# Kernel tuning notes

Measured on AMD Instinct MI355X. Metric: run time of the kernel, lower is better.

## Reference

```python
import jax, jax.numpy as jnp
import numpy as np

N_QUBITS = 12
N_LAYERS = 4
BATCH = 4096
DIM = 2 ** N_QUBITS  # 4096


def _apply_1q(state, U, q):
    """Apply 2x2 complex gate U to qubit q. state: (B,) + (2,)*n, wire 0 = MSB (axis q+1)."""
    state = jnp.moveaxis(state, q + 1, -1)
    state = state @ U.T
    return jnp.moveaxis(state, -1, q + 1)


def _apply_cnot(state, c, t):
    """CNOT with control c, target t: flip target amplitudes where control bit == 1."""
    flipped = jnp.flip(state, axis=t + 1)
    shape = [2 if i == c + 1 else 1 for i in range(state.ndim)]
    ctrl = jnp.arange(2).reshape(shape)
    return jnp.where(ctrl == 1, flipped, state)


def setup_inputs() -> dict:
    key = jax.random.key(0)
    k1, k2 = jax.random.split(key)
    x = jax.random.normal(k1, (BATCH, DIM), dtype=jnp.float32)
    weights = jax.random.normal(k2, (N_LAYERS, N_QUBITS, 2), dtype=jnp.float32) * 0.1
    return {"x": x, "weights": weights}


def reference(x, weights):
    n, L = N_QUBITS, N_LAYERS
    B = x.shape[0]
    # AmplitudeEmbedding with normalize=True
    norm = jnp.linalg.norm(x, axis=-1, keepdims=True)
    state = (x / norm).astype(jnp.complex64).reshape((B,) + (2,) * n)
    for layer in range(L):
        for q in range(n):
            ty = weights[layer, q, 0]
            tz = weights[layer, q, 1]
            c, s = jnp.cos(ty / 2), jnp.sin(ty / 2)
            em = jnp.exp(-0.5j * tz.astype(jnp.complex64))  # e^{-i tz/2}
            ep = jnp.exp(+0.5j * tz.astype(jnp.complex64))
            # U = RZ(tz) @ RY(ty), fused single 2x2 gate per qubit
            U = jnp.stack([
                jnp.stack([c * em, -s * em]),
                jnp.stack([s * ep, c * ep]),
            ]).astype(jnp.complex64)
            state = _apply_1q(state, U, q)
        for q in range(n - 1):
            state = _apply_cnot(state, q, q + 1)
        if n > 2:
            state = _apply_cnot(state, n - 1, 0)
    probs = jnp.abs(state) ** 2  # (B,) + (2,)*n, float32
    reduce_axes = tuple(range(1, probs.ndim))
    outs = []
    for q in range(n):
        shape = [2 if i == q + 1 else 1 for i in range(probs.ndim)]
        sign = jnp.array([1.0, -1.0], dtype=probs.dtype).reshape(shape)
        outs.append(jnp.sum(probs * sign, axis=reduce_axes))
    return jnp.stack(outs, axis=-1)  # (B, n_qubits) <Z_q> expvals
```

## Files before the change

### kernel.cpp

```cpp
#include <hip/hip_runtime.h>

#define NQ   12
#define DIM  4096
#define NL   4
#define BLK  256

typedef unsigned short u16;
typedef unsigned int   u32;
typedef float f2 __attribute__((ext_vector_type(2)));

struct L12 { u16 b[NQ]; };

static constexpr u32 lap(const L12& A, u32 x){ u32 r=0; for(int p=0;p<NQ;++p) if((x>>p)&1u) r^=A.b[p]; return r; }
static constexpr L12 lcomp(const L12& A, const L12& B){ L12 r{}; for(int p=0;p<NQ;++p) r.b[p]=(u16)lap(A,(u32)B.b[p]); return r; }
static constexpr L12 lident(){ L12 r{}; for(int p=0;p<NQ;++p) r.b[p]=(u16)(1u<<p); return r; }

static constexpr u32 applyT(u32 i){
  i ^= ((i>>0)&1u) << 11;
  for(int q=10;q>=0;--q){ int pc=11-q, pt=10-q; i ^= ((i>>pc)&1u) << pt; }
  return i;
}
static constexpr L12 lT(){ L12 t{}; for(int p=0;p<NQ;++p) t.b[p]=(u16)applyT(1u<<p); return t; }

static constexpr L12 linv(const L12& A){
  u16 v[NQ]; u16 u[NQ];
  for(int p=0;p<NQ;++p){ v[p]=A.b[p]; u[p]=(u16)(1u<<p); }
  for(int t=0;t<NQ;++t){
    int p=t; while(!((v[p]>>t)&1u)) ++p;
    u16 tv=v[p]; v[p]=v[t]; v[t]=tv; u16 tu=u[p]; u[p]=u[t]; u[t]=tu;
    for(int k=0;k<NQ;++k) if(k!=t && ((v[k]>>t)&1u)){ v[k]^=v[t]; u[k]^=u[t]; }
  }
  L12 r{}; for(int p=0;p<NQ;++p) r.b[p]=u[p]; return r;
}
static constexpr L12 ltr(const L12& A){
  L12 r{}; for(int p=0;p<NQ;++p) for(int q=0;q<NQ;++q) if((A.b[p]>>q)&1u) r.b[q]=(u16)(r.b[q]|(1u<<p));
  return r;
}
static constexpr int cpop(u32 v){ int n=0; while(v){ n+=(int)(v&1u); v>>=1; } return n; }

struct Tables {
  u16 cm[12][16];
  u16 wg[12][4];
  u16 sp[12][4];
  u16 wexp[NQ];
};

static constexpr Tables make_tables(){
  Tables tb{};
  const L12 T   = lT();
  const L12 Tit = ltr(linv(T));
  L12 A = lident();
  L12 W = lident();
  for(int l=0;l<NL;++l){
    for(int g=0;g<3;++g){
      const int st = l*3+g;
      u16 mm[4]={0,0,0,0};
      for(int i=0;i<4;++i){ mm[i]=A.b[4*g+i]; tb.wg[st][i]=W.b[4*g+i]; }
      u32 ech[4]={0,0,0,0}; int piv[4]={0,0,0,0};
      for(int i=0;i<4;++i){
        u32 v=mm[i];
        for(int k=0;k<i;++k) if((v>>piv[k])&1u) v^=ech[k];
        int t2=11; while(!((v>>t2)&1u)) --t2;
        piv[i]=t2; ech[i]=v;
      }
      for(int a2=0;a2<4;++a2) for(int b2=a2+1;b2<4;++b2)
        if(piv[b2]<piv[a2]){ int tt=piv[a2]; piv[a2]=piv[b2]; piv[b2]=tt; }
      for(int i=0;i<4;++i) tb.sp[st][i]=(u16)piv[i];
      for(int c=0;c<16;++c){ u32 m=0; for(int i=0;i<4;++i) if((c>>i)&1) m^=mm[i]; tb.cm[st][c]=(u16)m; }
    }
    A = lcomp(A, T);
    W = lcomp(W, Tit);
  }
  for(int p=0;p<NQ;++p) tb.wexp[p]=W.b[p];
  return tb;
}

__device__ constexpr Tables TB = make_tables();

static constexpr u16 UIMG[12] = {1,2,4,8, 3,5,6,7, 9,10,11,13};

static constexpr u32 swz(u32 j){
  u32 f=0;
  for(int k=4;k<12;++k) if((j>>k)&1u) f ^= (u32)UIMG[k];
  return j ^ (f & 15u);
}

struct Derived {
  u32 lane_c[12][8];
  u32 smb[12][4];
  u32 scmb[12][16];
  u32 g0lane[8];
  u32 u11lane[8];
  u32 u11smb[4];
  u16 pm[12];
  u16 mu[12];
};

static constexpr Derived make_derived(){
  const Tables tb = make_tables();
  Derived d{};
  for(int st=0; st<12; ++st){
    bool isp[12]={false,false,false,false,false,false,false,false,false,false,false,false};
    for(int i=0;i<4;++i) isp[tb.sp[st][i]]=true;
    int np[8]; int nn=0;
    for(int p=0;p<12;++p) if(!isp[p]) np[nn++]=p;
    int best=-1;
    for(int ms=0; ms<256; ++ms){
      int pc=0; for(int k=0;k<8;++k) pc+=(ms>>k)&1;
      if(pc!=6) continue;
      u16 bas[4]={0,0,0,0}; int r=0;
      for(int k=0;k<8;++k){
        if(!((ms>>k)&1)) continue;
        u16 x=(u16)(UIMG[np[k]]&15);
        while(x){
          int hb=3; while(!((x>>hb)&1)) --hb;
          if(bas[hb]) x=(u16)(x^bas[hb]);
          else { bas[hb]=x; ++r; x=0; }
        }
      }
      if(r==4){ best=ms; break; }
    }
    if(best<0) best=0x3F;
    int pos[8]; int lo=0, hi=6;
    for(int k=0;k<8;++k){ if((best>>k)&1) pos[lo++]=np[k]; else pos[hi++]=np[k]; }
    for(int k=0;k<8;++k){
      const u32 addr = swz(1u<<pos[k])<<3;
      u32 nib=0;
      for(int i=0;i<4;++i) nib |= (u32)((tb.wg[st][i]>>pos[k])&1u)<<i;
      d.lane_c[st][k] = addr | (nib<<28);
      if(st==0)  d.g0lane[k]  = 1u<<pos[k];
      if(st==11) d.u11lane[k] = 1u<<pos[k];
    }
    for(int i=0;i<4;++i)  d.smb[st][i]  = swz((u32)tb.cm[st][1<<i])<<3;
    for(int c=0;c<16;++c) d.scmb[st][c] = swz((u32)tb.cm[st][c])<<3;
    if(st==11) for(int i=0;i<4;++i) d.u11smb[i] = (u32)tb.cm[11][1<<i];
  }
  for(int q=0;q<12;++q){
    d.pm[q] = tb.wexp[11-q];
    u32 m=0;
    for(int i=0;i<4;++i) m |= (u32)(cpop((u32)tb.cm[11][1u<<i] & (u32)tb.wexp[11-q])&1)<<i;
    d.mu[q]=(u16)m;
  }
  return d;
}

__device__ constexpr Derived DV = make_derived();

template<int ST, bool WITHW>
__device__ __forceinline__ void gates(f2 (&a)[16], const float4* __restrict__ gw){
#pragma unroll
  for(int i=0;i<4;++i){
    const float4 g = gw[ST*4+i];
    const f2 mt = {-g.x, -g.x};
    const f2 sy = { g.y,  g.y};
#pragma unroll
    for(int c=0;c<16;++c){
      if((c>>i)&1) continue;
      const int c1 = c|(1<<i);
      f2 u = __builtin_elementwise_fma(mt, a[c1], a[c]);
      f2 v = __builtin_elementwise_fma(sy, u, a[c1]);
      a[c] = __builtin_elementwise_fma(mt, v, u);
      if(WITHW){
        const float t = fmaf(-g.z, v.y, v.x);
        v.y = fmaf( g.w, t, v.y);
        v.x = fmaf(-g.z, v.y, t);
      }
      a[c1]=v;
    }
  }
}

template<int ST, bool WITHW>
__device__ __forceinline__ void mid_step(const u32* msk, char* lds, const float4* __restrict__ gw){
  u32 acc=0;
#pragma unroll
  for(int k=0;k<8;++k) acc ^= DV.lane_c[ST][k]&msk[k];
  const u32 nib = acc>>28;
  u32 base = acc & 0x0FFFFFFFu;
#pragma unroll
  for(int i=0;i<4;++i) base ^= DV.smb[ST][i] & (0u-((nib>>i)&1u));
  u32 ad[16]; f2 a[16];
#pragma unroll
  for(int c=0;c<16;++c){
    ad[c] = base ^ DV.scmb[ST][c];
    a[c] = *(const f2*)(lds+ad[c]);
  }
  gates<ST,WITHW>(a,gw);
#pragma unroll
  for(int c=0;c<16;++c){ *(f2*)(lds+ad[c]) = a[c]; }
  __syncthreads();
}

__global__ void prep_kernel(const float* __restrict__ w, float4* __restrict__ gw){
  const int t = threadIdx.x;
  if(t < NL*NQ){
    const int l=t/NQ, p=t%NQ, q=(NQ-1)-p;
    const float ty=w[(l*NQ+q)*2+0], tz=w[(l*NQ+q)*2+1];
    gw[t]=make_float4(tanf(0.25f*ty), sinf(0.5f*ty), tanf(0.5f*tz), sinf(tz));
  }
}

__global__ __launch_bounds__(BLK, 5) void qsim_kernel(const float* __restrict__ x,
                                                      const float4* __restrict__ gw,
                                                      float* __restrict__ out)
{
  __shared__ f2 st2[DIM];
  char* lds = (char*)st2;
  const int tid = threadIdx.x;
  const int bb  = blockIdx.x;

  u32 msk[8];
#pragma unroll
  for(int k=0;k<8;++k) msk[k]=0u-((u32)(tid>>k)&1u);

  u32 rep0=0, acc0=0;
#pragma unroll
  for(int k=0;k<8;++k){ rep0 ^= DV.g0lane[k]&msk[k]; acc0 ^= DV.lane_c[0][k]&msk[k]; }
  const u32 base0 = acc0 & 0x0FFFFFFFu;

  f2 a[16];
  const float* xr = x + (size_t)bb*DIM + rep0;
#pragma unroll
  for(int s=0;s<4;++s){
    const float4 v = *reinterpret_cast<const float4*>(xr + 4*s);
    a[4*s+0]=(f2){v.x,0.f}; a[4*s+1]=(f2){v.y,0.f};
    a[4*s+2]=(f2){v.z,0.f}; a[4*s+3]=(f2){v.w,0.f};
  }
  gates<0,true>(a,gw);
#pragma unroll
  for(int c=0;c<16;++c){ *(f2*)(lds + (base0 ^ DV.scmb[0][c])) = a[c]; }
  __syncthreads();

  mid_step<1,true >(msk,lds,gw);
  mid_step<2,true >(msk,lds,gw);
  mid_step<3,true >(msk,lds,gw);
  mid_step<4,true >(msk,lds,gw);
  mid_step<5,true >(msk,lds,gw);
  mid_step<6,true >(msk,lds,gw);
  mid_step<7,true >(msk,lds,gw);
  mid_step<8,true >(msk,lds,gw);
  mid_step<9,false>(msk,lds,gw);
  mid_step<10,false>(msk,lds,gw);

  {
    u32 acc=0, urep=0;
#pragma unroll
    for(int k=0;k<8;++k){ acc ^= DV.lane_c[11][k]&msk[k]; urep ^= DV.u11lane[k]&msk[k]; }
    const u32 nib = acc>>28;
    u32 base = acc & 0x0FFFFFFFu;
#pragma unroll
    for(int i=0;i<4;++i){ const u32 mi=0u-((nib>>i)&1u); base ^= DV.smb[11][i]&mi; urep ^= DV.u11smb[i]&mi; }
#pragma unroll
    for(int c=0;c<16;++c){
      a[c] = *(const f2*)(lds + (base ^ DV.scmb[11][c]));
    }
    gates<11,false>(a,gw);

    float pr[16];
#pragma unroll
    for(int c=0;c<16;++c) pr[c]=fmaf(a[c].x,a[c].x, a[c].y*a[c].y);
#pragma unroll
    for(int b=1;b<16;b<<=1){
#pragma unroll
      for(int c=0;c<16;++c){
        if(c&b) continue;
        const float u=pr[c], v=pr[c|b];
        pr[c]=u+v; pr[c|b]=u-v;
      }
    }
    float accq[12];
#pragma unroll
    for(int q=0;q<12;++q){
      const u32 sb = ((u32)__popc(urep & (u32)DV.pm[q]) & 1u)<<31;
      accq[q]=__uint_as_float(__float_as_uint(pr[DV.mu[q]])^sb);
    }
    float nrm2 = pr[0];
#pragma unroll
    for(int o=32;o;o>>=1){
      nrm2 += __shfl_xor(nrm2,o);
#pragma unroll
      for(int q=0;q<12;++q) accq[q]+=__shfl_xor(accq[q],o);
    }
    __syncthreads();
    float* wredf = (float*)lds;
    const int wid=tid>>6;
    if((tid&63)==0){
#pragma unroll
      for(int q=0;q<12;++q) wredf[wid*13+q]=accq[q];
      wredf[wid*13+12]=nrm2;
    }
    __syncthreads();
    if(tid<NQ){
      const float s0=wredf[0*13+tid]+wredf[1*13+tid]+wredf[2*13+tid]+wredf[3*13+tid];
      const float sn=wredf[0*13+12]+wredf[1*13+12]+wredf[2*13+12]+wredf[3*13+12];
      out[(size_t)bb*NQ+tid]=s0/sn;
    }
  }
}

extern "C" void kernel_launch(void* const* d_in, const int* in_sizes, int n_in,
                              void* d_out, int out_size, void* d_ws, size_t ws_size,
                              hipStream_t stream) {
  const float* x = (const float*)d_in[0];
  const float* w = (const float*)d_in[1];
  float* out = (float*)d_out;
  float4* gw = (float4*)d_ws;
  const int B = in_sizes[0] / DIM;
  prep_kernel<<<1, 64, 0, stream>>>(w, gw);
  qsim_kernel<<<B, BLK, 0, stream>>>(x, gw, out);
}
```

Baseline: 107.0 us.

## Use packed FMA asm for RZ rotation and reorder lane bit selection

The scalar three-FMA RZ shear on each complex amplitude becomes three packed v_pk_fma_f32 instructions that use op_sel swizzles, with gate coefficients pre-broadcast into two float4 tables. The constexpr search that picks which state bits map to lanes now also requires a rank-3 condition on a subset, which changes the LDS address pattern, presumably to reduce bank conflicts. The launch bounds occupancy hint drops from 5 to 4 blocks, giving the compiler more registers. Together these aim to cut VALU instruction count and LDS conflict stalls, at the cost of inline asm and an extra coefficient load per gate.

```diff
diff --git a/kernel.cpp b/kernel.cpp
--- a/kernel.cpp
+++ b/kernel.cpp
@@ -75,14 +75,24 @@
   return tb;
 }
 
-__device__ constexpr Tables TB = make_tables();
-
 static constexpr u16 UIMG[12] = {1,2,4,8, 3,5,6,7, 9,10,11,13};
 
 static constexpr u32 swz(u32 j){
   u32 f=0;
   for(int k=4;k<12;++k) if((j>>k)&1u) f ^= (u32)UIMG[k];
   return j ^ (f & 15u);
+}
+
+static constexpr int rankbits(const u16* v, int n, u16 mask){
+  u16 bas[4]={0,0,0,0}; int r=0;
+  for(int i=0;i<n;++i){
+    u16 x=(u16)(v[i]&mask);
+    for(int it=0; it<5 && x; ++it){
+      int hb=3; while(hb>0 && !((x>>hb)&1u)) --hb;
+      if(bas[hb]) x=(u16)(x^bas[hb]); else { bas[hb]=x; ++r; x=0; }
+    }
+  }
+  return r;
 }
 
 struct Derived {
@@ -104,32 +114,37 @@
     for(int i=0;i<4;++i) isp[tb.sp[st][i]]=true;
     int np[8]; int nn=0;
     for(int p=0;p<12;++p) if(!isp[p]) np[nn++]=p;
-    int best=-1;
-    for(int ms=0; ms<256; ++ms){
-      int pc=0; for(int k=0;k<8;++k) pc+=(ms>>k)&1;
-      if(pc!=6) continue;
-      u16 bas[4]={0,0,0,0}; int r=0;
-      for(int k=0;k<8;++k){
-        if(!((ms>>k)&1)) continue;
-        u16 x=(u16)(UIMG[np[k]]&15);
-        while(x){
-          int hb=3; while(!((x>>hb)&1)) --hb;
-          if(bas[hb]) x=(u16)(x^bas[hb]);
-          else { bas[hb]=x; ++r; x=0; }
+    u16 img8[8];
+    for(int j=0;j<8;++j) img8[j]=(u16)(swz(1u<<np[j])&15u);
+    int ord[8]={0,1,2,3,4,5,6,7}; bool okf=false;
+    for(int a=0;a<8&&!okf;++a)for(int b=a+1;b<8&&!okf;++b)
+    for(int c2=b+1;c2<8&&!okf;++c2)for(int dd=c2+1;dd<8&&!okf;++dd){
+      u16 four[4]={img8[a],img8[b],img8[c2],img8[dd]};
+      if(rankbits(four,4,15)!=4) continue;
+      const int ids[4]={a,b,c2,dd};
+      for(int ex=0; ex<4 && !okf; ++ex){
+        u16 tri[3]; int tj=0;
+        for(int j=0;j<4;++j) if(j!=ex) tri[tj++]=four[j];
+        if(rankbits(tri,3,7)!=3) continue;
+        int pp=0;
+        for(int j=0;j<4;++j) if(j!=ex) ord[pp++]=ids[j];
+        ord[3]=ids[ex];
+        int rp=4;
+        for(int j=0;j<8;++j){
+          bool used=false; for(int k2=0;k2<4;++k2) if(ids[k2]==j) used=true;
+          if(!used) ord[rp++]=j;
         }
+        okf=true;
       }
-      if(r==4){ best=ms; break; }
-    }
-    if(best<0) best=0x3F;
-    int pos[8]; int lo=0, hi=6;
-    for(int k=0;k<8;++k){ if((best>>k)&1) pos[lo++]=np[k]; else pos[hi++]=np[k]; }
+    }
     for(int k=0;k<8;++k){
-      const u32 addr = swz(1u<<pos[k])<<3;
+      const int pos = np[ord[k]];
+      const u32 addr = swz(1u<<pos)<<3;
       u32 nib=0;
-      for(int i=0;i<4;++i) nib |= (u32)((tb.wg[st][i]>>pos[k])&1u)<<i;
+      for(int i=0;i<4;++i) nib |= (u32)((tb.wg[st][i]>>pos)&1u)<<i;
       d.lane_c[st][k] = addr | (nib<<28);
-      if(st==0)  d.g0lane[k]  = 1u<<pos[k];
-      if(st==11) d.u11lane[k] = 1u<<pos[k];
+      if(st==0)  d.g0lane[k]  = 1u<<pos;
+      if(st==11) d.u11lane[k] = 1u<<pos;
     }
     for(int i=0;i<4;++i)  d.smb[st][i]  = swz((u32)tb.cm[st][1<<i])<<3;
     for(int c=0;c<16;++c) d.scmb[st][c] = swz((u32)tb.cm[st][c])<<3;
@@ -146,24 +161,49 @@
 
 __device__ constexpr Derived DV = make_derived();
 
+__device__ __forceinline__ f2 pkfma(f2 a, f2 b, f2 c){
+  f2 d;
+  asm("v_pk_fma_f32 %0, %1, %2, %3" : "=v"(d) : "v"(a), "v"(b), "v"(c));
+  return d;
+}
+__device__ __forceinline__ f2 pkswz1(f2 v, f2 b){
+  f2 d;
+  asm("v_pk_fma_f32 %0, %1, %2, %3 op_sel:[1,0,0] op_sel_hi:[1,1,1]"
+      : "=v"(d) : "v"(v), "v"(b), "v"(v));
+  return d;
+}
+__device__ __forceinline__ f2 pkswz2(f2 v, f2 b){
+  f2 d;
+  asm("v_pk_fma_f32 %0, %1, %2, %3 op_sel:[0,0,0] op_sel_hi:[0,1,1]"
+      : "=v"(d) : "v"(v), "v"(b), "v"(v));
+  return d;
+}
+
 template<int ST, bool WITHW>
-__device__ __forceinline__ void gates(f2 (&a)[16], const float4* __restrict__ gw){
+__device__ __forceinline__ void gates(f2 (&a)[16], const float4* __restrict__ gwA,
+                                      const float4* __restrict__ gwB){
 #pragma unroll
   for(int i=0;i<4;++i){
-    const float4 g = gw[ST*4+i];
-    const f2 mt = {-g.x, -g.x};
-    const f2 sy = { g.y,  g.y};
+    const float4 A = gwA[ST*4+i];
+    const f2 mt = {A.x, A.y};
+    const f2 sy = {A.z, A.w};
+    f2 bz1, bz2;
+    if(WITHW){
+      const float4 B = gwB[ST*4+i];
+      bz1 = (f2){B.x, B.y};
+      bz2 = (f2){B.z, B.w};
+    }
 #pragma unroll
     for(int c=0;c<16;++c){
       if((c>>i)&1) continue;
       const int c1 = c|(1<<i);
-      f2 u = __builtin_elementwise_fma(mt, a[c1], a[c]);
-      f2 v = __builtin_elementwise_fma(sy, u, a[c1]);
-      a[c] = __builtin_elementwise_fma(mt, v, u);
+      f2 u = pkfma(a[c1], mt, a[c]);
+      f2 v = pkfma(u, sy, a[c1]);
+      a[c] = pkfma(v, mt, u);
       if(WITHW){
-        const float t = fmaf(-g.z, v.y, v.x);
-        v.y = fmaf( g.w, t, v.y);
-        v.x = fmaf(-g.z, v.y, t);
+        v = pkswz1(v, bz1);
+        v = pkswz2(v, bz2);
+        v = pkswz1(v, bz1);
       }
       a[c1]=v;
     }
@@ -171,7 +211,9 @@
 }
 
 template<int ST, bool WITHW>
-__device__ __forceinline__ void mid_step(const u32* msk, char* lds, const float4* __restrict__ gw){
+__device__ __forceinline__ void mid_step(const u32* msk, char* lds,
+                                         const float4* __restrict__ gwA,
+                                         const float4* __restrict__ gwB){
   u32 acc=0;
 #pragma unroll
   for(int k=0;k<8;++k) acc ^= DV.lane_c[ST][k]&msk[k];
@@ -185,23 +227,27 @@
     ad[c] = base ^ DV.scmb[ST][c];
     a[c] = *(const f2*)(lds+ad[c]);
   }
-  gates<ST,WITHW>(a,gw);
+  gates<ST,WITHW>(a,gwA,gwB);
 #pragma unroll
   for(int c=0;c<16;++c){ *(f2*)(lds+ad[c]) = a[c]; }
   __syncthreads();
 }
 
-__global__ void prep_kernel(const float* __restrict__ w, float4* __restrict__ gw){
+__global__ void prep_kernel(const float* __restrict__ w, float4* __restrict__ gwA,
+                            float4* __restrict__ gwB){
   const int t = threadIdx.x;
   if(t < NL*NQ){
     const int l=t/NQ, p=t%NQ, q=(NQ-1)-p;
     const float ty=w[(l*NQ+q)*2+0], tz=w[(l*NQ+q)*2+1];
-    gw[t]=make_float4(tanf(0.25f*ty), sinf(0.5f*ty), tanf(0.5f*tz), sinf(tz));
-  }
-}
-
-__global__ __launch_bounds__(BLK, 5) void qsim_kernel(const float* __restrict__ x,
-                                                      const float4* __restrict__ gw,
+    const float mt=-tanf(0.25f*ty), sy=sinf(0.5f*ty);
+    gwA[t]=make_float4(mt, mt, sy, sy);
+    gwB[t]=make_float4(-tanf(0.5f*tz), 0.f, 0.f, sinf(tz));
+  }
+}
+
+__global__ __launch_bounds__(BLK, 4) void qsim_kernel(const float* __restrict__ x,
+                                                      const float4* __restrict__ gwA,
+                                                      const float4* __restrict__ gwB,
                                                       float* __restrict__ out)
 {
   __shared__ f2 st2[DIM];
@@ -226,21 +272,21 @@
     a[4*s+0]=(f2){v.x,0.f}; a[4*s+1]=(f2){v.y,0.f};
     a[4*s+2]=(f2){v.z,0.f}; a[4*s+3]=(f2){v.w,0.f};
   }
-  gates<0,true>(a,gw);
+  gates<0,true>(a,gwA,gwB);
 #pragma unroll
   for(int c=0;c<16;++c){ *(f2*)(lds + (base0 ^ DV.scmb[0][c])) = a[c]; }
   __syncthreads();
 
-  mid_step<1,true >(msk,lds,gw);
-  mid_step<2,true >(msk,lds,gw);
-  mid_step<3,true >(msk,lds,gw);
-  mid_step<4,true >(msk,lds,gw);
-  mid_step<5,true >(msk,lds,gw);
-  mid_step<6,true >(msk,lds,gw);
-  mid_step<7,true >(msk,lds,gw);
-  mid_step<8,true >(msk,lds,gw);
-  mid_step<9,false>(msk,lds,gw);
-  mid_step<10,false>(msk,lds,gw);
+  mid_step<1,true >(msk,lds,gwA,gwB);
+  mid_step<2,true >(msk,lds,gwA,gwB);
+  mid_step<3,true >(msk,lds,gwA,gwB);
+  mid_step<4,true >(msk,lds,gwA,gwB);
+  mid_step<5,true >(msk,lds,gwA,gwB);
+  mid_step<6,true >(msk,lds,gwA,gwB);
+  mid_step<7,true >(msk,lds,gwA,gwB);
+  mid_step<8,true >(msk,lds,gwA,gwB);
+  mid_step<9,false>(msk,lds,gwA,gwB);
+  mid_step<10,false>(msk,lds,gwA,gwB);
 
   {
     u32 acc=0, urep=0;
@@ -254,7 +300,7 @@
     for(int c=0;c<16;++c){
       a[c] = *(const f2*)(lds + (base ^ DV.scmb[11][c]));
     }
-    gates<11,false>(a,gw);
+    gates<11,false>(a,gwA,gwB);
 
     float pr[16];
 #pragma unroll
@@ -304,8 +350,9 @@
   const float* x = (const float*)d_in[0];
   const float* w = (const float*)d_in[1];
   float* out = (float*)d_out;
-  float4* gw = (float4*)d_ws;
+  float4* gwA = (float4*)d_ws;
+  float4* gwB = gwA + NL*NQ;
   const int B = in_sizes[0] / DIM;
-  prep_kernel<<<1, 64, 0, stream>>>(w, gw);
-  qsim_kernel<<<B, BLK, 0, stream>>>(x, gw, out);
-}
+  prep_kernel<<<1, 64, 0, stream>>>(w, gwA, gwB);
+  qsim_kernel<<<B, BLK, 0, stream>>>(x, gwA, gwB, out);
+}
```

Result: slower. 121.9 us (+13.9%).
